# Optimization experiments

Hardware: AMD Instinct MI355X
Metric: run time of the kernel (lower is better)

Reference implementation:

```python
import jax, jax.numpy as jnp
import numpy as np

N_NODES = 100000
N_EDGES = 1600000
NFEAT = 256
NCLASS = 2


def setup_inputs() -> dict:
    key = jax.random.key(0)
    ks = jax.random.split(key, 16)
    x = jax.random.normal(ks[0], (N_NODES, NFEAT), dtype=jnp.float32)
    row = jax.random.randint(ks[1], (N_EDGES,), 0, N_NODES, dtype=jnp.int64) if jax.config.jax_enable_x64 else jax.random.randint(ks[1], (N_EDGES,), 0, N_NODES, dtype=jnp.int32)
    col = jax.random.randint(ks[2], (N_EDGES,), 0, N_NODES, dtype=row.dtype)
    edge_val = jax.random.uniform(ks[3], (N_EDGES,), dtype=jnp.float32)

    def unif(k, shape, fan_out):
        stdv = 1.0 / np.sqrt(fan_out)
        return jax.random.uniform(k, shape, dtype=jnp.float32, minval=-stdv, maxval=stdv)

    W1 = unif(ks[4], (NFEAT, 32), 32); b1 = unif(ks[5], (32,), 32)
    W2 = unif(ks[6], (32, 48), 48);   b2 = unif(ks[7], (48,), 48)
    W3 = unif(ks[8], (48, 64), 64);   b3 = unif(ks[9], (64,), 64)
    fc1_W = unif(ks[10], (64, 32), 64); fc1_b = unif(ks[11], (32,), 64)
    fc2_W = unif(ks[12], (32, NCLASS), 32); fc2_b = unif(ks[13], (NCLASS,), 32)
    return {"x": x, "row": row, "col": col, "edge_val": edge_val,
            "W1": W1, "b1": b1, "W2": W2, "b2": b2, "W3": W3, "b3": b3,
            "fc1_W": fc1_W, "fc1_b": fc1_b, "fc2_W": fc2_W, "fc2_b": fc2_b}


def _spmm(row, col, val, dense):
    # out[i] = sum_{e: row[e]==i} val[e] * dense[col[e]]   (COO sparse @ dense)
    gathered = dense[col] * val[:, None]          # [E, F]
    return jax.ops.segment_sum(gathered, row, num_segments=N_NODES)


def _gc_layer(x, row, col, val, W, b):
    support = x @ W                               # dense mm  [N, out]
    return _spmm(row, col, val, support) + b      # spmm + bias


def reference(x, row, col, edge_val, W1, b1, W2, b2, W3, b3, fc1_W, fc1_b, fc2_W, fc2_b):
    # eval mode: dropout is identity
    h = jax.nn.relu(_gc_layer(x, row, col, edge_val, W1, b1))   # [N, 32]
    h = jax.nn.relu(_gc_layer(h, row, col, edge_val, W2, b2))   # [N, 48]
    h = jax.nn.relu(_gc_layer(h, row, col, edge_val, W3, b3))   # [N, 64]
    y = jnp.mean(h, axis=0)                                     # [64] global mean pool
    y = jax.nn.relu(y @ fc1_W + fc1_b)                          # [32]
    y = jax.nn.softmax(y @ fc2_W + fc2_b, axis=0)               # [nclass]
    return y
```

## Files before the change

kernel.cpp:

```cpp
#include <hip/hip_runtime.h>
#include <hip/hip_bf16.h>

#define N_NODES 100000
#define N_EDGES 1600000

#define NT 391
#define NB1 128
#define CHUNK ((N_EDGES + NB1 - 1) / NB1)
#define ROWS3 40
#define GRID3 (N_NODES / ROWS3)
#define GB1 ((N_NODES + 63) / 64)

typedef __attribute__((ext_vector_type(8))) short bf16x8;
typedef __attribute__((ext_vector_type(4))) float f32x4;

__device__ __forceinline__ unsigned char f2q(float f) {
    return (unsigned char)(__builtin_amdgcn_cvt_pk_fp8_f32(f, f, 0, false) & 0xFF);
}
__device__ __forceinline__ unsigned pack4_fp8(float a0, float a1, float a2, float a3) {
    int r = __builtin_amdgcn_cvt_pk_fp8_f32(a0, a1, 0, false);
    r = __builtin_amdgcn_cvt_pk_fp8_f32(a2, a3, r, true);
    return (unsigned)r;
}
__device__ __forceinline__ unsigned short f2bf(float f) {
    unsigned u = __float_as_uint(f);
    u += 0x7FFFu + ((u >> 16) & 1u);
    return (unsigned short)(u >> 16);
}
#define CVT(u, s) __builtin_amdgcn_cvt_f32_fp8((u), (s))

#define ACC4(A, U, V)                                                               \
    A[0] += (V) * CVT((U), 0); A[1] += (V) * CVT((U), 1);                           \
    A[2] += (V) * CVT((U), 2); A[3] += (V) * CVT((U), 3);

#define ACC8(A, U, V)                                                               \
    A[0] += (V) * CVT((U).x, 0); A[1] += (V) * CVT((U).x, 1);                       \
    A[2] += (V) * CVT((U).x, 2); A[3] += (V) * CVT((U).x, 3);                       \
    A[4] += (V) * CVT((U).y, 0); A[5] += (V) * CVT((U).y, 1);                       \
    A[6] += (V) * CVT((U).y, 2); A[7] += (V) * CVT((U).y, 3);

__global__ __launch_bounds__(256) void k_wprep(const float* __restrict__ W,
                                               unsigned short* __restrict__ wb) {
    int kk = blockIdx.x >> 1, t = blockIdx.x & 1;
    int tid = threadIdx.x;
    for (int i = tid; i < 512; i += 256) {
        int l = i >> 3, j = i & 7;
        int k = kk * 32 + ((l >> 4) << 3) + j;
        int c = t * 16 + (l & 15);
        wb[(size_t)(blockIdx.x * 64 + l) * 8 + j] = f2bf(W[(size_t)k * 32 + c]);
    }
}

__global__ __launch_bounds__(256) void k_gemm1_phist(const float* __restrict__ x,
                                                     const unsigned short* __restrict__ wb,
                                                     unsigned char* __restrict__ out,
                                                     const int* __restrict__ row, int* __restrict__ blkhist) {
    __shared__ __align__(16) char smem[64 * 72 * 2];
    int tid = threadIdx.x;
    if (blockIdx.x >= GB1) {
        int* h = (int*)smem;
        int b = blockIdx.x - GB1;
        for (int i = tid; i < NT; i += 256) h[i] = 0;
        __syncthreads();
        int s = b * CHUNK, e = min(s + CHUNK, N_EDGES);
        for (int i = s + tid; i < e; i += 256) atomicAdd(&h[row[i] >> 8], 1);
        __syncthreads();
        for (int i = tid; i < NT; i += 256) blkhist[i * NB1 + b] = h[i];
        return;
    }
    unsigned short (*XA)[72] = (unsigned short(*)[72])smem;
    int bn = blockIdx.x * 64;
    int lane = tid & 63;
    int wbase = (tid >> 6) * 16;
    f32x4 acc0 = {0.f, 0.f, 0.f, 0.f};
    f32x4 acc1 = {0.f, 0.f, 0.f, 0.f};
    for (int kc = 0; kc < 4; ++kc) {
        if (kc) __syncthreads();
        #pragma unroll
        for (int i = 0; i < 4; ++i) {
            int idx = i * 256 + tid;
            int n = idx >> 4;
            int k4 = (idx & 15) * 4;
            float4 v = make_float4(0.f, 0.f, 0.f, 0.f);
            if (bn + n < N_NODES)
                v = *reinterpret_cast<const float4*>(&x[(size_t)(bn + n) * 256 + kc * 64 + k4]);
            ushort4 b;
            b.x = f2bf(v.x); b.y = f2bf(v.y); b.z = f2bf(v.z); b.w = f2bf(v.w);
            *reinterpret_cast<ushort4*>(&XA[n][k4]) = b;
        }
        __syncthreads();
        bf16x8 bf[2][2];
        #pragma unroll
        for (int ks = 0; ks < 2; ++ks)
            #pragma unroll
            for (int t = 0; t < 2; ++t)
                bf[ks][t] = *reinterpret_cast<const bf16x8*>(
                    &wb[(size_t)((((kc * 2 + ks) * 2) + t) * 64 + lane) * 8]);
        #pragma unroll
        for (int ks = 0; ks < 2; ++ks) {
            bf16x8 af = *reinterpret_cast<const bf16x8*>(
                &XA[wbase + (lane & 15)][ks * 32 + ((lane >> 4) << 3)]);
            acc0 = __builtin_amdgcn_mfma_f32_16x16x32_bf16(af, bf[ks][0], acc0, 0, 0, 0);
            acc1 = __builtin_amdgcn_mfma_f32_16x16x32_bf16(af, bf[ks][1], acc1, 0, 0, 0);
        }
    }
    #pragma unroll
    for (int r = 0; r < 4; ++r) {
        int n = bn + wbase + ((lane >> 4) << 2) + r;
        if (n < N_NODES) {
            out[(size_t)n * 32 + (lane & 15)]      = f2q(acc0[r]);
            out[(size_t)n * 32 + 16 + (lane & 15)] = f2q(acc1[r]);
        }
    }
}


__global__ __launch_bounds__(128) void k_bscan1(int* __restrict__ blkhist, int* __restrict__ cnt) {
    __shared__ int s[128];
    int j = blockIdx.x, t = threadIdx.x;
    int v = blkhist[j * NB1 + t];
    s[t] = v;
    __syncthreads();
    #pragma unroll
    for (int st = 1; st < 128; st <<= 1) {
        int u = (t >= st) ? s[t - st] : 0;
        __syncthreads();
        s[t] += u;
        __syncthreads();
    }
    blkhist[j * NB1 + t] = s[t] - v;
    if (t == 127) cnt[j] = s[127];
}

__global__ __launch_bounds__(512) void k_bscan2(const int* __restrict__ cnt, int* __restrict__ base,
                                                int* __restrict__ row_ptr) {
    __shared__ int s[512];
    int j = threadIdx.x;
    int v = (j < NT) ? cnt[j] : 0;
    s[j] = v;
    __syncthreads();
    for (int st = 1; st < 512; st <<= 1) {
        int u = (j >= st) ? s[j - st] : 0;
        __syncthreads();
        s[j] += u;
        __syncthreads();
    }
    if (j < NT) base[j] = s[j] - v;
    if (j == 0) row_ptr[N_NODES] = N_EDGES;
}

__global__ __launch_bounds__(256) void k_pscatter(const int* __restrict__ row, const int* __restrict__ col,
                                                  const float* __restrict__ val,
                                                  const int* __restrict__ blkhist, const int* __restrict__ base,
                                                  int2* __restrict__ part) {
    __shared__ int cur[NT];
    int b = blockIdx.x, t = threadIdx.x;
    for (int i = t; i < NT; i += 256) cur[i] = blkhist[i * NB1 + b] + base[i];
    __syncthreads();
    int s = b * CHUNK, e = min(s + CHUNK, N_EDGES);
    for (int i = s + t; i < e; i += 256) {
        int r = row[i];
        int j = r >> 8;
        int p = atomicAdd(&cur[j], 1);
        part[p] = make_int2(((r & 255) << 24) | col[i], __float_as_int(val[i]));
    }
}

__global__ __launch_bounds__(256) void k_sort(const int2* __restrict__ part, const int* __restrict__ cnt,
                                              const int* __restrict__ base, int* __restrict__ row_ptr,
                                              unsigned* __restrict__ csr) {
    __shared__ int hist[256];
    __shared__ int cur[256];
    int b = blockIdx.x, t = threadIdx.x;
    int n = cnt[b];
    int bb = base[b];
    const int2* sl = part + bb;
    hist[t] = 0;
    __syncthreads();
    for (int i = t; i < n; i += 256) atomicAdd(&hist[((unsigned)sl[i].x) >> 24], 1);
    __syncthreads();
    int v = hist[t];
    for (int st = 1; st < 256; st <<= 1) {
        int u = (t >= st) ? hist[t - st] : 0;
        __syncthreads();
        hist[t] += u;
        __syncthreads();
    }
    cur[t] = hist[t] - v;
    int grow = b * 256 + t;
    if (grow < N_NODES) row_ptr[grow] = bb + cur[t];
    __syncthreads();
    for (int i = t; i < n; i += 256) {
        int2 e = sl[i];
        int rl = ((unsigned)e.x) >> 24;
        int p = atomicAdd(&cur[rl], 1);
        unsigned c = (unsigned)(e.x & 0xFFFFFF);
        float vf = __int_as_float(e.y);
        int q = __float2int_rn(vf * 32768.0f);
        if (q > 32767) q = 32767;
        csr[bb + p] = (c << 15) | (unsigned)q;
    }
}

__global__ __launch_bounds__(256, 8) void k_spmm1(const int* __restrict__ rp, const unsigned* __restrict__ csr,
                                                  const unsigned char* __restrict__ sup,
                                                  const float* __restrict__ bias,
                                                  unsigned char* __restrict__ out) {
    int gid = blockIdx.x * 256 + threadIdx.x;
    int n = gid >> 3;
    if (n >= N_NODES) return;
    int f4 = (gid & 7) * 4;
    int e0 = rp[n], e1 = rp[n + 1];
    float a[4] = {};
    int e = e0;
    if ((e & 1) && e < e1) {
        unsigned ent = csr[e];
        float v = (float)(ent & 0x7FFF);
        unsigned u = *reinterpret_cast<const unsigned*>(&sup[(size_t)(ent >> 15) * 32 + f4]);
        ACC4(a, u, v)
        ++e;
    }
    for (; e + 1 < e1; e += 2) {
        uint2 p = *reinterpret_cast<const uint2*>(&csr[e]);
        unsigned u0 = *reinterpret_cast<const unsigned*>(&sup[(size_t)(p.x >> 15) * 32 + f4]);
        unsigned u1 = *reinterpret_cast<const unsigned*>(&sup[(size_t)(p.y >> 15) * 32 + f4]);
        float v0 = (float)(p.x & 0x7FFF), v1 = (float)(p.y & 0x7FFF);
        ACC4(a, u0, v0)
        ACC4(a, u1, v1)
    }
    if (e < e1) {
        unsigned ent = csr[e];
        float v = (float)(ent & 0x7FFF);
        unsigned u = *reinterpret_cast<const unsigned*>(&sup[(size_t)(ent >> 15) * 32 + f4]);
        ACC4(a, u, v)
    }
    const float sc = 1.0f / 32768.0f;
    unsigned r = pack4_fp8(fmaxf(a[0] * sc + bias[f4 + 0], 0.f), fmaxf(a[1] * sc + bias[f4 + 1], 0.f),
                           fmaxf(a[2] * sc + bias[f4 + 2], 0.f), fmaxf(a[3] * sc + bias[f4 + 3], 0.f));
    *reinterpret_cast<unsigned*>(&out[(size_t)n * 32 + f4]) = r;
}

__global__ __launch_bounds__(256, 8) void k_l2fused(const int* __restrict__ rp, const unsigned* __restrict__ csr,
                                                    const unsigned char* __restrict__ h1,
                                                    const float* __restrict__ W2, const float* __restrict__ b2,
                                                    unsigned char* __restrict__ h2) {
    __shared__ float w2s[32 * 48];
    __shared__ float b2s[48];
    __shared__ float g2s[32][33];
    int tid = threadIdx.x;
    for (int i = tid; i < 32 * 48; i += 256) w2s[i] = W2[i];
    if (tid < 48) b2s[tid] = b2[tid];
    int n0 = blockIdx.x * 32;
    int grp = tid >> 3;
    int f4 = (tid & 7) * 4;
    int n = n0 + grp;
    {
        int e0 = rp[n], e1 = rp[n + 1];
        float a[4] = {};
        int e = e0;
        if ((e & 1) && e < e1) {
            unsigned ent = csr[e];
            float v = (float)(ent & 0x7FFF);
            unsigned u = *reinterpret_cast<const unsigned*>(&h1[(size_t)(ent >> 15) * 32 + f4]);
            ACC4(a, u, v)
            ++e;
        }
        for (; e + 1 < e1; e += 2) {
            uint2 p = *reinterpret_cast<const uint2*>(&csr[e]);
            unsigned u0 = *reinterpret_cast<const unsigned*>(&h1[(size_t)(p.x >> 15) * 32 + f4]);
            unsigned u1 = *reinterpret_cast<const unsigned*>(&h1[(size_t)(p.y >> 15) * 32 + f4]);
            float v0 = (float)(p.x & 0x7FFF), v1 = (float)(p.y & 0x7FFF);
            ACC4(a, u0, v0)
            ACC4(a, u1, v1)
        }
        if (e < e1) {
            unsigned ent = csr[e];
            float v = (float)(ent & 0x7FFF);
            unsigned u = *reinterpret_cast<const unsigned*>(&h1[(size_t)(ent >> 15) * 32 + f4]);
            ACC4(a, u, v)
        }
        const float sc = 1.0f / 32768.0f;
        g2s[grp][f4 + 0] = a[0] * sc;
        g2s[grp][f4 + 1] = a[1] * sc;
        g2s[grp][f4 + 2] = a[2] * sc;
        g2s[grp][f4 + 3] = a[3] * sc;
    }
    __syncthreads();
    #pragma unroll
    for (int pp = 0; pp < 6; ++pp) {
        int idx = pp * 256 + tid;
        int r = idx / 48;
        int m = idx - 48 * r;
        float a = b2s[m];
        const float* g = g2s[r];
        #pragma unroll
        for (int k = 0; k < 32; ++k) a += g[k] * w2s[k * 48 + m];
        h2[(size_t)(n0 + r) * 48 + m] = f2q(fmaxf(a, 0.f));
    }
}

__global__ __launch_bounds__(256, 7) void k_l3fused(const int* __restrict__ rp, const unsigned* __restrict__ csr,
                                                    const unsigned char* __restrict__ h2,
                                                    const float* __restrict__ W3, const float* __restrict__ b3,
                                                    float* __restrict__ poolpart) {
    __shared__ float w3s[48 * 64];
    __shared__ float b3s[64];
    __shared__ float g3s[ROWS3][49];
    __shared__ float red[256];
    int tid = threadIdx.x;
    for (int i = tid; i < 48 * 64; i += 256) w3s[i] = W3[i];
    if (tid < 64) b3s[tid] = b3[tid];
    int grp = tid / 6;
    int f8 = (tid - grp * 6) * 8;
    int m = tid & 63;
    const float sc = 1.0f / 32768.0f;
    if (tid < 240) {
        int n = blockIdx.x * ROWS3 + grp;
        int e0 = rp[n], e1 = rp[n + 1];
        float a[8] = {};
        int e = e0;
        if ((e & 1) && e < e1) {
            unsigned ent = csr[e];
            float v = (float)(ent & 0x7FFF);
            uint2 u = *reinterpret_cast<const uint2*>(&h2[(size_t)(ent >> 15) * 48 + f8]);
            ACC8(a, u, v)
            ++e;
        }
        for (; e + 1 < e1; e += 2) {
            uint2 p = *reinterpret_cast<const uint2*>(&csr[e]);
            uint2 u0 = *reinterpret_cast<const uint2*>(&h2[(size_t)(p.x >> 15) * 48 + f8]);
            uint2 u1 = *reinterpret_cast<const uint2*>(&h2[(size_t)(p.y >> 15) * 48 + f8]);
            float v0 = (float)(p.x & 0x7FFF), v1 = (float)(p.y & 0x7FFF);
            ACC8(a, u0, v0)
            ACC8(a, u1, v1)
        }
        if (e < e1) {
            unsigned ent = csr[e];
            float v = (float)(ent & 0x7FFF);
            uint2 u = *reinterpret_cast<const uint2*>(&h2[(size_t)(ent >> 15) * 48 + f8]);
            ACC8(a, u, v)
        }
        #pragma unroll
        for (int j = 0; j < 8; ++j) g3s[grp][f8 + j] = a[j] * sc;
    }
    __syncthreads();
    float poolacc = 0.f;
    #pragma unroll
    for (int pp = 0; pp < 10; ++pp) {
        int r = 4 * pp + (tid >> 6);
        float a = b3s[m];
        const float* gg = g3s[r];
        #pragma unroll
        for (int k = 0; k < 48; ++k) a += gg[k] * w3s[k * 64 + m];
        poolacc += fmaxf(a, 0.f);
    }
    red[tid] = poolacc;
    __syncthreads();
    if (tid < 64) {
        float s = red[tid] + red[tid + 64] + red[tid + 128] + red[tid + 192];
        poolpart[(size_t)blockIdx.x * 64 + tid] = s;
    }
}

__global__ __launch_bounds__(256) void k_preduce(const float* __restrict__ poolpart,
                                                 float* __restrict__ pool) {
    __shared__ float red[256];
    int b = blockIdx.x, t = threadIdx.x;
    float s = 0.f;
    for (int j = t; j < GRID3; j += 256) s += poolpart[(size_t)j * 64 + b];
    red[t] = s;
    __syncthreads();
    for (int st = 128; st > 0; st >>= 1) {
        if (t < st) red[t] += red[t + st];
        __syncthreads();
    }
    if (t == 0) pool[b] = red[0];
}

__global__ __launch_bounds__(64) void k_head(const float* __restrict__ pool,
                                             const float* __restrict__ fc1W, const float* __restrict__ fc1b,
                                             const float* __restrict__ fc2W, const float* __restrict__ fc2b,
                                             float* __restrict__ out) {
    __shared__ float pl[64];
    __shared__ float z[32];
    __shared__ float lg[2];
    int t = threadIdx.x;
    pl[t] = pool[t] * (1.0f / (float)N_NODES);
    __syncthreads();
    if (t < 32) {
        float a = fc1b[t];
        #pragma unroll
        for (int o = 0; o < 64; ++o) a += pl[o] * fc1W[o * 32 + t];
        z[t] = fmaxf(a, 0.f);
    }
    __syncthreads();
    if (t < 2) {
        float l = fc2b[t];
        #pragma unroll
        for (int j = 0; j < 32; ++j) l += z[j] * fc2W[j * 2 + t];
        lg[t] = l;
    }
    __syncthreads();
    if (t == 0) {
        float mx = fmaxf(lg[0], lg[1]);
        float e0 = __expf(lg[0] - mx), e1 = __expf(lg[1] - mx);
        float ss = e0 + e1;
        out[0] = e0 / ss;
        out[1] = e1 / ss;
    }
}


extern "C" void kernel_launch(void* const* d_in, const int* in_sizes, int n_in,
                              void* d_out, int out_size, void* d_ws, size_t ws_size,
                              hipStream_t stream) {
    const float* x    = (const float*)d_in[0];
    const int*   row  = (const int*)d_in[1];
    const int*   col  = (const int*)d_in[2];
    const float* val  = (const float*)d_in[3];
    const float* W1   = (const float*)d_in[4];
    const float* b1   = (const float*)d_in[5];
    const float* W2   = (const float*)d_in[6];
    const float* b2   = (const float*)d_in[7];
    const float* W3   = (const float*)d_in[8];
    const float* b3   = (const float*)d_in[9];
    const float* fc1W = (const float*)d_in[10];
    const float* fc1b = (const float*)d_in[11];
    const float* fc2W = (const float*)d_in[12];
    const float* fc2b = (const float*)d_in[13];
    float* out = (float*)d_out;

    char* wsb = (char*)d_ws;
    size_t off = 0;
    auto alloc = [&](size_t bytes) {
        void* p = wsb + off;
        off += (bytes + 255) / 256 * 256;
        return p;
    };
    int*      blkhist  = (int*)alloc((size_t)NT * NB1 * 4);
    int*      base     = (int*)alloc((size_t)NT * 4);
    int*      cnt      = (int*)alloc((size_t)NT * 4);
    int*      row_ptr  = (int*)alloc((size_t)(N_NODES + 1) * 4);
    int2*     part     = (int2*)alloc((size_t)N_EDGES * 8);
    unsigned* csr      = (unsigned*)alloc((size_t)N_EDGES * 4);
    unsigned char* sup = (unsigned char*)alloc((size_t)N_NODES * 32);
    unsigned char* h1  = (unsigned char*)alloc((size_t)N_NODES * 32);
    unsigned char* h2  = (unsigned char*)alloc((size_t)N_NODES * 48);
    float* poolpart    = (float*)alloc((size_t)GRID3 * 64 * 4);
    float* pool        = (float*)alloc(64 * 4);
    unsigned short* wb = (unsigned short*)alloc((size_t)16 * 64 * 8 * 2);

    k_wprep<<<16, 256, 0, stream>>>(W1, wb);
    k_gemm1_phist<<<GB1 + NB1, 256, 0, stream>>>(x, wb, sup, row, blkhist);
    k_bscan1<<<NT, 128, 0, stream>>>(blkhist, cnt);
    k_bscan2<<<1, 512, 0, stream>>>(cnt, base, row_ptr);
    k_pscatter<<<NB1, 256, 0, stream>>>(row, col, val, blkhist, base, part);
    k_sort<<<NT, 256, 0, stream>>>(part, cnt, base, row_ptr, csr);

    k_spmm1<<<(N_NODES * 8 + 255) / 256, 256, 0, stream>>>(row_ptr, csr, sup, b1, h1);
    k_l2fused<<<(N_NODES + 31) / 32, 256, 0, stream>>>(row_ptr, csr, h1, W2, b2, h2);
    k_l3fused<<<GRID3, 256, 0, stream>>>(row_ptr, csr, h2, W3, b3, poolpart);
    k_preduce<<<64, 256, 0, stream>>>(poolpart, pool);
    k_head<<<1, 64, 0, stream>>>(pool, fc1W, fc1b, fc2W, fc2b, out);
}
```

Before: 197.0 us.

## Split partition buffer into packed col/val and row-byte arrays; widen SpMM lanes to 8 features

The partition scatter now quantizes the edge value and packs it with the column into one 32-bit word. The local row goes into a separate byte array, replacing the 8-byte int2 staging buffer, which cuts scatter and sort traffic from 8 to 5 bytes per edge. The sort pass then only copies the packed word. The layer-1 and layer-2 SpMM kernels now give each thread 8 fp8 features via 8-byte loads instead of 4, halving the threads per node and doubling the nodes per block in the fused layer-2 kernel, with new bounds checks. This trades more registers per thread and fewer threads for fewer, wider gathers and less redundant csr and row_ptr reading.

```diff
diff --git a/kernel.cpp b/kernel.cpp
--- a/kernel.cpp
+++ b/kernel.cpp
@@ -28,10 +28,6 @@
     return (unsigned short)(u >> 16);
 }
 #define CVT(u, s) __builtin_amdgcn_cvt_f32_fp8((u), (s))
-
-#define ACC4(A, U, V)                                                               \
-    A[0] += (V) * CVT((U), 0); A[1] += (V) * CVT((U), 1);                           \
-    A[2] += (V) * CVT((U), 2); A[3] += (V) * CVT((U), 3);
 
 #define ACC8(A, U, V)                                                               \
     A[0] += (V) * CVT((U).x, 0); A[1] += (V) * CVT((U).x, 1);                       \
@@ -152,7 +148,7 @@
 __global__ __launch_bounds__(256) void k_pscatter(const int* __restrict__ row, const int* __restrict__ col,
                                                   const float* __restrict__ val,
                                                   const int* __restrict__ blkhist, const int* __restrict__ base,
-                                                  int2* __restrict__ part) {
+                                                  unsigned* __restrict__ pcv, unsigned char* __restrict__ prl) {
     __shared__ int cur[NT];
     int b = blockIdx.x, t = threadIdx.x;
     for (int i = t; i < NT; i += 256) cur[i] = blkhist[i * NB1 + b] + base[i];
@@ -162,11 +158,16 @@
         int r = row[i];
         int j = r >> 8;
         int p = atomicAdd(&cur[j], 1);
-        part[p] = make_int2(((r & 255) << 24) | col[i], __float_as_int(val[i]));
-    }
-}
-
-__global__ __launch_bounds__(256) void k_sort(const int2* __restrict__ part, const int* __restrict__ cnt,
+        int q = __float2int_rn(val[i] * 32768.0f);
+        if (q > 32767) q = 32767;
+        pcv[p] = ((unsigned)col[i] << 15) | (unsigned)q;
+        prl[p] = (unsigned char)(r & 255);
+    }
+}
+
+__global__ __launch_bounds__(256) void k_sort(const unsigned* __restrict__ pcv,
+                                              const unsigned char* __restrict__ prl,
+                                              const int* __restrict__ cnt,
                                               const int* __restrict__ base, int* __restrict__ row_ptr,
                                               unsigned* __restrict__ csr) {
     __shared__ int hist[256];
@@ -174,10 +175,9 @@
     int b = blockIdx.x, t = threadIdx.x;
     int n = cnt[b];
     int bb = base[b];
-    const int2* sl = part + bb;
     hist[t] = 0;
     __syncthreads();
-    for (int i = t; i < n; i += 256) atomicAdd(&hist[((unsigned)sl[i].x) >> 24], 1);
+    for (int i = t; i < n; i += 256) atomicAdd(&hist[prl[bb + i]], 1);
     __syncthreads();
     int v = hist[t];
     for (int st = 1; st < 256; st <<= 1) {
@@ -191,14 +191,9 @@
     if (grow < N_NODES) row_ptr[grow] = bb + cur[t];
     __syncthreads();
     for (int i = t; i < n; i += 256) {
-        int2 e = sl[i];
-        int rl = ((unsigned)e.x) >> 24;
+        int rl = prl[bb + i];
         int p = atomicAdd(&cur[rl], 1);
-        unsigned c = (unsigned)(e.x & 0xFFFFFF);
-        float vf = __int_as_float(e.y);
-        int q = __float2int_rn(vf * 32768.0f);
-        if (q > 32767) q = 32767;
-        csr[bb + p] = (c << 15) | (unsigned)q;
+        csr[bb + p] = pcv[bb + i];
     }
 }
 
@@ -207,37 +202,40 @@
                                                   const float* __restrict__ bias,
                                                   unsigned char* __restrict__ out) {
     int gid = blockIdx.x * 256 + threadIdx.x;
-    int n = gid >> 3;
+    int n = gid >> 2;
     if (n >= N_NODES) return;
-    int f4 = (gid & 7) * 4;
+    int f8 = (gid & 3) * 8;
     int e0 = rp[n], e1 = rp[n + 1];
-    float a[4] = {};
+    float a[8] = {};
     int e = e0;
     if ((e & 1) && e < e1) {
         unsigned ent = csr[e];
         float v = (float)(ent & 0x7FFF);
-        unsigned u = *reinterpret_cast<const unsigned*>(&sup[(size_t)(ent >> 15) * 32 + f4]);
-        ACC4(a, u, v)
+        uint2 u = *reinterpret_cast<const uint2*>(&sup[(size_t)(ent >> 15) * 32 + f8]);
+        ACC8(a, u, v)
         ++e;
     }
     for (; e + 1 < e1; e += 2) {
         uint2 p = *reinterpret_cast<const uint2*>(&csr[e]);
-        unsigned u0 = *reinterpret_cast<const unsigned*>(&sup[(size_t)(p.x >> 15) * 32 + f4]);
-        unsigned u1 = *reinterpret_cast<const unsigned*>(&sup[(size_t)(p.y >> 15) * 32 + f4]);
+        uint2 u0 = *reinterpret_cast<const uint2*>(&sup[(size_t)(p.x >> 15) * 32 + f8]);
+        uint2 u1 = *reinterpret_cast<const uint2*>(&sup[(size_t)(p.y >> 15) * 32 + f8]);
         float v0 = (float)(p.x & 0x7FFF), v1 = (float)(p.y & 0x7FFF);
-        ACC4(a, u0, v0)
-        ACC4(a, u1, v1)
+        ACC8(a, u0, v0)
+        ACC8(a, u1, v1)
     }
     if (e < e1) {
         unsigned ent = csr[e];
         float v = (float)(ent & 0x7FFF);
-        unsigned u = *reinterpret_cast<const unsigned*>(&sup[(size_t)(ent >> 15) * 32 + f4]);
-        ACC4(a, u, v)
+        uint2 u = *reinterpret_cast<const uint2*>(&sup[(size_t)(ent >> 15) * 32 + f8]);
+        ACC8(a, u, v)
     }
     const float sc = 1.0f / 32768.0f;
-    unsigned r = pack4_fp8(fmaxf(a[0] * sc + bias[f4 + 0], 0.f), fmaxf(a[1] * sc + bias[f4 + 1], 0.f),
-                           fmaxf(a[2] * sc + bias[f4 + 2], 0.f), fmaxf(a[3] * sc + bias[f4 + 3], 0.f));
-    *reinterpret_cast<unsigned*>(&out[(size_t)n * 32 + f4]) = r;
+    uint2 r;
+    r.x = pack4_fp8(fmaxf(a[0] * sc + bias[f8 + 0], 0.f), fmaxf(a[1] * sc + bias[f8 + 1], 0.f),
+                    fmaxf(a[2] * sc + bias[f8 + 2], 0.f), fmaxf(a[3] * sc + bias[f8 + 3], 0.f));
+    r.y = pack4_fp8(fmaxf(a[4] * sc + bias[f8 + 4], 0.f), fmaxf(a[5] * sc + bias[f8 + 5], 0.f),
+                    fmaxf(a[6] * sc + bias[f8 + 6], 0.f), fmaxf(a[7] * sc + bias[f8 + 7], 0.f));
+    *reinterpret_cast<uint2*>(&out[(size_t)n * 32 + f8]) = r;
 }
 
 __global__ __launch_bounds__(256, 8) void k_l2fused(const int* __restrict__ rp, const unsigned* __restrict__ csr,
@@ -246,56 +244,56 @@
                                                     unsigned char* __restrict__ h2) {
     __shared__ float w2s[32 * 48];
     __shared__ float b2s[48];
-    __shared__ float g2s[32][33];
+    __shared__ float g2s[64][33];
     int tid = threadIdx.x;
     for (int i = tid; i < 32 * 48; i += 256) w2s[i] = W2[i];
     if (tid < 48) b2s[tid] = b2[tid];
-    int n0 = blockIdx.x * 32;
-    int grp = tid >> 3;
-    int f4 = (tid & 7) * 4;
+    int n0 = blockIdx.x * 64;
+    int grp = tid >> 2;
+    int f8 = (tid & 3) * 8;
     int n = n0 + grp;
-    {
+    if (n < N_NODES) {
         int e0 = rp[n], e1 = rp[n + 1];
-        float a[4] = {};
+        float a[8] = {};
         int e = e0;
         if ((e & 1) && e < e1) {
             unsigned ent = csr[e];
             float v = (float)(ent & 0x7FFF);
-            unsigned u = *reinterpret_cast<const unsigned*>(&h1[(size_t)(ent >> 15) * 32 + f4]);
-            ACC4(a, u, v)
+            uint2 u = *reinterpret_cast<const uint2*>(&h1[(size_t)(ent >> 15) * 32 + f8]);
+            ACC8(a, u, v)
             ++e;
         }
         for (; e + 1 < e1; e += 2) {
             uint2 p = *reinterpret_cast<const uint2*>(&csr[e]);
-            unsigned u0 = *reinterpret_cast<const unsigned*>(&h1[(size_t)(p.x >> 15) * 32 + f4]);
-            unsigned u1 = *reinterpret_cast<const unsigned*>(&h1[(size_t)(p.y >> 15) * 32 + f4]);
+            uint2 u0 = *reinterpret_cast<const uint2*>(&h1[(size_t)(p.x >> 15) * 32 + f8]);
+            uint2 u1 = *reinterpret_cast<const uint2*>(&h1[(size_t)(p.y >> 15) * 32 + f8]);
             float v0 = (float)(p.x & 0x7FFF), v1 = (float)(p.y & 0x7FFF);
-            ACC4(a, u0, v0)
-            ACC4(a, u1, v1)
+            ACC8(a, u0, v0)
+            ACC8(a, u1, v1)
         }
         if (e < e1) {
             unsigned ent = csr[e];
             float v = (float)(ent & 0x7FFF);
-            unsigned u = *reinterpret_cast<const unsigned*>(&h1[(size_t)(ent >> 15) * 32 + f4]);
-            ACC4(a, u, v)
+            uint2 u = *reinterpret_cast<const uint2*>(&h1[(size_t)(ent >> 15) * 32 + f8]);
+            ACC8(a, u, v)
         }
         const float sc = 1.0f / 32768.0f;
-        g2s[grp][f4 + 0] = a[0] * sc;
-        g2s[grp][f4 + 1] = a[1] * sc;
-        g2s[grp][f4 + 2] = a[2] * sc;
-        g2s[grp][f4 + 3] = a[3] * sc;
+        #pragma unroll
+        for (int j = 0; j < 8; ++j) g2s[grp][f8 + j] = a[j] * sc;
     }
     __syncthreads();
     #pragma unroll
-    for (int pp = 0; pp < 6; ++pp) {
+    for (int pp = 0; pp < 12; ++pp) {
         int idx = pp * 256 + tid;
         int r = idx / 48;
         int m = idx - 48 * r;
-        float a = b2s[m];
-        const float* g = g2s[r];
-        #pragma unroll
-        for (int k = 0; k < 32; ++k) a += g[k] * w2s[k * 48 + m];
-        h2[(size_t)(n0 + r) * 48 + m] = f2q(fmaxf(a, 0.f));
+        if (n0 + r < N_NODES) {
+            float a = b2s[m];
+            const float* g = g2s[r];
+            #pragma unroll
+            for (int k = 0; k < 32; ++k) a += g[k] * w2s[k * 48 + m];
+            h2[(size_t)(n0 + r) * 48 + m] = f2q(fmaxf(a, 0.f));
+        }
     }
 }
 
@@ -441,7 +439,8 @@
     int*      base     = (int*)alloc((size_t)NT * 4);
     int*      cnt      = (int*)alloc((size_t)NT * 4);
     int*      row_ptr  = (int*)alloc((size_t)(N_NODES + 1) * 4);
-    int2*     part     = (int2*)alloc((size_t)N_EDGES * 8);
+    unsigned* pcv      = (unsigned*)alloc((size_t)N_EDGES * 4);
+    unsigned char* prl = (unsigned char*)alloc((size_t)N_EDGES);
     unsigned* csr      = (unsigned*)alloc((size_t)N_EDGES * 4);
     unsigned char* sup = (unsigned char*)alloc((size_t)N_NODES * 32);
     unsigned char* h1  = (unsigned char*)alloc((size_t)N_NODES * 32);
@@ -454,11 +453,11 @@
     k_gemm1_phist<<<GB1 + NB1, 256, 0, stream>>>(x, wb, sup, row, blkhist);
     k_bscan1<<<NT, 128, 0, stream>>>(blkhist, cnt);
     k_bscan2<<<1, 512, 0, stream>>>(cnt, base, row_ptr);
-    k_pscatter<<<NB1, 256, 0, stream>>>(row, col, val, blkhist, base, part);
-    k_sort<<<NT, 256, 0, stream>>>(part, cnt, base, row_ptr, csr);
-
-    k_spmm1<<<(N_NODES * 8 + 255) / 256, 256, 0, stream>>>(row_ptr, csr, sup, b1, h1);
-    k_l2fused<<<(N_NODES + 31) / 32, 256, 0, stream>>>(row_ptr, csr, h1, W2, b2, h2);
+    k_pscatter<<<NB1, 256, 0, stream>>>(row, col, val, blkhist, base, pcv, prl);
+    k_sort<<<NT, 256, 0, stream>>>(pcv, prl, cnt, base, row_ptr, csr);
+
+    k_spmm1<<<(N_NODES * 4 + 255) / 256, 256, 0, stream>>>(row_ptr, csr, sup, b1, h1);
+    k_l2fused<<<(N_NODES + 63) / 64, 256, 0, stream>>>(row_ptr, csr, h1, W2, b2, h2);
     k_l3fused<<<GRID3, 256, 0, stream>>>(row_ptr, csr, h2, W3, b3, poolpart);
     k_preduce<<<64, 256, 0, stream>>>(poolpart, pool);
     k_head<<<1, 64, 0, stream>>>(pool, fc1W, fc1b, fc2W, fc2b, out);
```

After: 206.1 us. 1.05x slower.
